# Kernel optimization log

Measured on AMD Instinct MI355X. Metric: run time of the kernel, lower is better.

## Reference

```python
import jax, jax.numpy as jnp
import numpy as np

B, S, D = 4, 2048, 1024
H = 16
HD = D // H  # head_dim = 64


def setup_inputs() -> dict:
    key = jax.random.key(0)
    ks = jax.random.split(key, 8)
    scale = 1.0 / np.sqrt(D)
    return {
        "X_Q": jax.random.normal(ks[0], (B, S, D), dtype=jnp.float32),
        "X_KV": jax.random.normal(ks[1], (B, S, D), dtype=jnp.float32),
        # q_proj: Linear(D, D), weights stored as (in, out)
        "q_w": jax.random.normal(ks[2], (D, D), dtype=jnp.float32) * scale,
        "q_b": jax.random.normal(ks[3], (D,), dtype=jnp.float32) * scale,
        # kv_proj: Linear(D, 2*D)
        "kv_w": jax.random.normal(ks[4], (D, 2 * D), dtype=jnp.float32) * scale,
        "kv_b": jax.random.normal(ks[5], (2 * D,), dtype=jnp.float32) * scale,
        # out_proj: Linear(D, D) (query_dim == input_dim)
        "out_w": jax.random.normal(ks[6], (D, D), dtype=jnp.float32) * scale,
        "out_b": jax.random.normal(ks[7], (D,), dtype=jnp.float32) * scale,
    }


def reference(X_Q, X_KV, q_w, q_b, kv_w, kv_b, out_w, out_b):
    # projections
    q = X_Q @ q_w + q_b                      # [b, s, D]
    kv = X_KV @ kv_w + kv_b                  # [b, l, 2D]
    k, v = jnp.split(kv, 2, axis=-1)         # each [b, l, D]

    def split_heads(t):
        b, m, _ = t.shape
        return t.reshape(b, m, H, HD).transpose(0, 2, 1, 3)  # [b, h, m, d]

    q, k, v = split_heads(q), split_heads(k), split_heads(v)

    # standard attention: full SxL scores (non-flash path)
    scores = jnp.einsum("bhsd,bhld->bhsl", q, k) / np.sqrt(HD)
    attn = jax.nn.softmax(scores, axis=-1)   # dropout_p = 0 -> identity
    out = jnp.einsum("bhsl,bhld->bhsd", attn, v)

    # merge heads: [b, h, s, d] -> [b, s, h*d]
    out = out.transpose(0, 2, 1, 3).reshape(B, S, D)
    return out @ out_w + out_b
```

## Files before the change

kernel.cpp:

```cpp
#include <hip/hip_runtime.h>
#include <hip/hip_bf16.h>
#include <math.h>

#define B_  4
#define S_  2048
#define D_  1024
#define H_  16
#define HD_ 64

typedef __bf16 bf16;
typedef __bf16 bf16x4 __attribute__((ext_vector_type(4)));
typedef __bf16 bf16x8 __attribute__((ext_vector_type(8)));
typedef float  floatx4 __attribute__((ext_vector_type(4)));
typedef unsigned short ushort8 __attribute__((ext_vector_type(8)));

#define QSCALE 0.18033688011112042f

__global__ __launch_bounds__(256) void cast_f32_bf16(
    const float* __restrict__ in, bf16* __restrict__ out, int n) {
  int i = (blockIdx.x * blockDim.x + threadIdx.x) * 4;
  if (i >= n) return;
  float4 v = *reinterpret_cast<const float4*>(in + i);
  bf16x4 o;
  o[0] = (bf16)v.x; o[1] = (bf16)v.y; o[2] = (bf16)v.z; o[3] = (bf16)v.w;
  *reinterpret_cast<bf16x4*>(out + i) = o;
}

__global__ __launch_bounds__(256) void transcast(
    const float* __restrict__ in, bf16* __restrict__ out, int K, int N) {
  __shared__ float tile[32][33];
  int k0 = blockIdx.y * 32, n0 = blockIdx.x * 32;
  int tx = threadIdx.x, ty = threadIdx.y;
  #pragma unroll
  for (int i = ty; i < 32; i += 8)
    tile[i][tx] = in[(size_t)(k0 + i) * N + n0 + tx];
  __syncthreads();
  #pragma unroll
  for (int i = ty; i < 32; i += 8)
    out[(size_t)(n0 + i) * K + k0 + tx] = (bf16)tile[tx][i];
}

template <int MODE>
__global__ __launch_bounds__(256) void gemm_bt(
    const bf16* __restrict__ A, const bf16* __restrict__ Bt,
    const float* __restrict__ bias, void* __restrict__ out,
    int M, int N, int K) {
  __shared__ bf16 As[128][72];
  __shared__ bf16 Bs[128][72];

  const int tid  = threadIdx.x;
  const int m0   = blockIdx.y * 128;
  const int n0   = blockIdx.x * 128;
  const int w    = tid >> 6;
  const int lane = tid & 63;
  const int lr   = lane & 15;
  const int lq   = lane >> 4;
  const int wm   = (w >> 1) * 64;
  const int wn   = (w & 1) * 64;

  floatx4 acc[4][4];
  #pragma unroll
  for (int i = 0; i < 4; i++)
    #pragma unroll
    for (int j = 0; j < 4; j++)
      acc[i][j] = floatx4{0.f, 0.f, 0.f, 0.f};

  const int rA = tid >> 3;
  const int cA = (tid & 7) * 8;

  for (int k0 = 0; k0 < K; k0 += 64) {
    __syncthreads();
    #pragma unroll
    for (int p = 0; p < 4; p++) {
      int r = rA + p * 32;
      *reinterpret_cast<ushort8*>(&As[r][cA]) =
          *reinterpret_cast<const ushort8*>(A + (size_t)(m0 + r) * K + k0 + cA);
      *reinterpret_cast<ushort8*>(&Bs[r][cA]) =
          *reinterpret_cast<const ushort8*>(Bt + (size_t)(n0 + r) * K + k0 + cA);
    }
    __syncthreads();
    #pragma unroll
    for (int kc = 0; kc < 2; kc++) {
      bf16x8 af[4], bfv[4];
      #pragma unroll
      for (int t = 0; t < 4; t++)
        af[t] = *reinterpret_cast<const bf16x8*>(&As[wm + 16 * t + lr][kc * 32 + lq * 8]);
      #pragma unroll
      for (int t = 0; t < 4; t++)
        bfv[t] = *reinterpret_cast<const bf16x8*>(&Bs[wn + 16 * t + lr][kc * 32 + lq * 8]);
      #pragma unroll
      for (int i = 0; i < 4; i++)
        #pragma unroll
        for (int j = 0; j < 4; j++)
          acc[i][j] = __builtin_amdgcn_mfma_f32_16x16x32_bf16(af[i], bfv[j], acc[i][j], 0, 0, 0);
    }
  }

  #pragma unroll
  for (int i = 0; i < 4; i++) {
    int row_base = m0 + wm + 16 * i + lq * 4;
    #pragma unroll
    for (int j = 0; j < 4; j++) {
      int col = n0 + wn + 16 * j + lr;
      float bv = bias[col];
      if (MODE == 2 && col >= 1024) {
        int b = row_base >> 11, s0 = row_base & 2047;
        int c = col - 1024, h = c >> 6, d = c & 63;
        bf16* Vt = (bf16*)out + (size_t)B_ * H_ * S_ * HD_;
        bf16x4 pk;
        #pragma unroll
        for (int r = 0; r < 4; r++) pk[r] = (bf16)(acc[i][j][r] + bv);
        *reinterpret_cast<bf16x4*>(
            &Vt[(((size_t)b * H_ + h) * HD_ + d) * S_ + s0]) = pk;
        continue;
      }
      #pragma unroll
      for (int r = 0; r < 4; r++) {
        int row = row_base + r;
        float v = acc[i][j][r] + bv;
        if (MODE == 0) {
          ((float*)out)[(size_t)row * N + col] = v;
        } else if (MODE == 1) {
          int b = row >> 11, s = row & 2047;
          int h = col >> 6, d = col & 63;
          ((bf16*)out)[(((size_t)b * H_ + h) * S_ + s) * HD_ + d] =
              (bf16)(v * QSCALE);
        } else {
          int b = row >> 11, s = row & 2047;
          int h = col >> 6, d = col & 63;
          ((bf16*)out)[(((size_t)b * H_ + h) * S_ + s) * HD_ + d] = (bf16)v;
        }
      }
    }
  }
}

__global__ __launch_bounds__(256) void attn_kernel(
    const bf16* __restrict__ Q, const bf16* __restrict__ Kb,
    const bf16* __restrict__ Vt, bf16* __restrict__ out) {
  __shared__ bf16 qs[64][72];
  __shared__ bf16 ks[64][72];
  __shared__ bf16 vts[64][72];
  __shared__ bf16 ps[4][16][72];

  const int tid  = threadIdx.x;
  const int w    = tid >> 6;
  const int lane = tid & 63;
  const int lr   = lane & 15;
  const int lq   = lane >> 4;
  const int q0   = blockIdx.x * 64;
  const int bh   = blockIdx.y;
  const size_t base = (size_t)bh * S_ * HD_;

  const int rS = tid >> 3;
  const int cS = (tid & 7) * 8;

  #pragma unroll
  for (int p = 0; p < 2; p++)
    *reinterpret_cast<ushort8*>(&qs[rS + 32 * p][cS]) =
        *reinterpret_cast<const ushort8*>(Q + base + (size_t)(q0 + rS + 32 * p) * HD_ + cS);
  __syncthreads();

  bf16x8 bq[2];
  #pragma unroll
  for (int kc = 0; kc < 2; kc++)
    bq[kc] = *reinterpret_cast<const bf16x8*>(&qs[16 * w + lr][kc * 32 + lq * 8]);

  float l_i = 0.f;
  floatx4 o_acc[4];
  #pragma unroll
  for (int t = 0; t < 4; t++) o_acc[t] = floatx4{0.f, 0.f, 0.f, 0.f};

  for (int l0 = 0; l0 < S_; l0 += 64) {
    __syncthreads();
    #pragma unroll
    for (int p = 0; p < 2; p++) {
      int r = rS + 32 * p;
      *reinterpret_cast<ushort8*>(&ks[r][cS]) =
          *reinterpret_cast<const ushort8*>(Kb + base + (size_t)(l0 + r) * HD_ + cS);
      *reinterpret_cast<ushort8*>(&vts[r][cS]) =
          *reinterpret_cast<const ushort8*>(Vt + base + (size_t)r * S_ + l0 + cS);
    }
    __syncthreads();

    floatx4 sc[4];
    #pragma unroll
    for (int t = 0; t < 4; t++) sc[t] = floatx4{0.f, 0.f, 0.f, 0.f};
    #pragma unroll
    for (int kc = 0; kc < 2; kc++) {
      #pragma unroll
      for (int t = 0; t < 4; t++) {
        bf16x8 ak = *reinterpret_cast<const bf16x8*>(&ks[16 * t + lr][kc * 32 + lq * 8]);
        sc[t] = __builtin_amdgcn_mfma_f32_16x16x32_bf16(ak, bq[kc], sc[t], 0, 0, 0);
      }
    }

    float lsum = 0.f;
    #pragma unroll
    for (int t = 0; t < 4; t++) {
      bf16x4 pk;
      #pragma unroll
      for (int r = 0; r < 4; r++) {
        float p = __builtin_amdgcn_exp2f(sc[t][r]);
        lsum += p;
        pk[r] = (bf16)p;
      }
      *reinterpret_cast<bf16x4*>(&ps[w][lr][16 * t + lq * 4]) = pk;
    }
    l_i += lsum;
    __builtin_amdgcn_wave_barrier();

    #pragma unroll
    for (int kc = 0; kc < 2; kc++) {
      bf16x8 bp = *reinterpret_cast<const bf16x8*>(&ps[w][lr][kc * 32 + lq * 8]);
      #pragma unroll
      for (int t = 0; t < 4; t++) {
        bf16x8 av = *reinterpret_cast<const bf16x8*>(&vts[16 * t + lr][kc * 32 + lq * 8]);
        o_acc[t] = __builtin_amdgcn_mfma_f32_16x16x32_bf16(av, bp, o_acc[t], 0, 0, 0);
      }
    }
  }

  l_i += __shfl_xor(l_i, 16, 64);
  l_i += __shfl_xor(l_i, 32, 64);
  float inv = 1.0f / l_i;

  const int b = bh >> 4, h = bh & 15;
  const int qrow = q0 + 16 * w + lr;
  bf16* orow = out + ((size_t)b * S_ + qrow) * D_ + h * HD_;
  #pragma unroll
  for (int t = 0; t < 4; t++) {
    bf16x4 pk;
    #pragma unroll
    for (int r = 0; r < 4; r++) pk[r] = (bf16)(o_acc[t][r] * inv);
    *reinterpret_cast<bf16x4*>(&orow[16 * t + lq * 4]) = pk;
  }
}

extern "C" void kernel_launch(void* const* d_in, const int* in_sizes, int n_in,
                              void* d_out, int out_size, void* d_ws, size_t ws_size,
                              hipStream_t stream) {
  const float* X_Q   = (const float*)d_in[0];
  const float* X_KV  = (const float*)d_in[1];
  const float* q_w   = (const float*)d_in[2];
  const float* q_b   = (const float*)d_in[3];
  const float* kv_w  = (const float*)d_in[4];
  const float* kv_b  = (const float*)d_in[5];
  const float* out_w = (const float*)d_in[6];
  const float* out_b = (const float*)d_in[7];
  float* out = (float*)d_out;

  char* ws = (char*)d_ws;
  const size_t MB = 1024 * 1024;
  bf16* Xq   = (bf16*)(ws + 0);
  bf16* Xkv  = (bf16*)(ws + 16 * MB);
  bf16* Qb   = (bf16*)(ws + 32 * MB);
  bf16* Kb   = (bf16*)(ws + 48 * MB);
  bf16* qwT  = (bf16*)(ws + 80 * MB);
  bf16* kvwT = (bf16*)(ws + 82 * MB);
  bf16* owT  = (bf16*)(ws + 86 * MB);
  bf16* Vt   = Kb + (size_t)B_ * H_ * S_ * HD_;
  bf16* attn = Xq;

  const int nX = B_ * S_ * D_;

  cast_f32_bf16<<<nX / 1024, 256, 0, stream>>>(X_Q, Xq, nX);
  cast_f32_bf16<<<nX / 1024, 256, 0, stream>>>(X_KV, Xkv, nX);
  transcast<<<dim3(32, 32), dim3(32, 8), 0, stream>>>(q_w, qwT, 1024, 1024);
  transcast<<<dim3(64, 32), dim3(32, 8), 0, stream>>>(kv_w, kvwT, 1024, 2048);
  transcast<<<dim3(32, 32), dim3(32, 8), 0, stream>>>(out_w, owT, 1024, 1024);

  gemm_bt<1><<<dim3(8, 64), 256, 0, stream>>>(Xq, qwT, q_b, Qb, 8192, 1024, 1024);
  gemm_bt<2><<<dim3(16, 64), 256, 0, stream>>>(Xkv, kvwT, kv_b, Kb, 8192, 2048, 1024);
  attn_kernel<<<dim3(32, 64), 256, 0, stream>>>(Qb, Kb, Vt, attn);
  gemm_bt<0><<<dim3(8, 64), 256, 0, stream>>>(attn, owT, out_b, out, 8192, 1024, 1024);
}
```

Baseline: 373.0 us.

## Use direct global-to-LDS loads with XOR swizzle and 128-query attention tiles

Both the GEMM and attention kernels now load global data straight into LDS with global_load_lds, which skips the register round trip. LDS tiles drop their padding and use an XOR swizzle to avoid bank conflicts. The attention kernel now handles 128 query rows per block, two 16-row groups per wave, so each K/V tile feeds twice the MFMA work. It also reuses the Q smem region as the per-wave P buffer and adds a launch-bounds occupancy hint. The risks are more register pressure and that the synchronisation of the async loads relies only on __syncthreads.

Result: faster. 336.9 us (-9.7%).

```diff
diff --git a/kernel.cpp b/kernel.cpp
--- a/kernel.cpp
+++ b/kernel.cpp
@@ -15,6 +15,12 @@
 typedef unsigned short ushort8 __attribute__((ext_vector_type(8)));
 
 #define QSCALE 0.18033688011112042f
+
+__device__ __forceinline__ void async_load16(const bf16* g, bf16* l) {
+  __builtin_amdgcn_global_load_lds(
+      (const __attribute__((address_space(1))) void*)g,
+      (__attribute__((address_space(3))) void*)l, 16, 0, 0);
+}
 
 __global__ __launch_bounds__(256) void cast_f32_bf16(
     const float* __restrict__ in, bf16* __restrict__ out, int n) {
@@ -45,8 +51,8 @@
     const bf16* __restrict__ A, const bf16* __restrict__ Bt,
     const float* __restrict__ bias, void* __restrict__ out,
     int M, int N, int K) {
-  __shared__ bf16 As[128][72];
-  __shared__ bf16 Bs[128][72];
+  __shared__ bf16 As[128][64];
+  __shared__ bf16 Bs[128][64];
 
   const int tid  = threadIdx.x;
   const int m0   = blockIdx.y * 128;
@@ -58,6 +64,11 @@
   const int wm   = (w >> 1) * 64;
   const int wn   = (w & 1) * 64;
 
+  const int srow = lane >> 3;
+  const int sg   = (lane & 7) ^ srow;
+  const bf16* aptr = A  + (size_t)(m0 + 32 * w + srow) * K + 8 * sg;
+  const bf16* bptr = Bt + (size_t)(n0 + 32 * w + srow) * K + 8 * sg;
+
   floatx4 acc[4][4];
   #pragma unroll
   for (int i = 0; i < 4; i++)
@@ -65,29 +76,24 @@
     for (int j = 0; j < 4; j++)
       acc[i][j] = floatx4{0.f, 0.f, 0.f, 0.f};
 
-  const int rA = tid >> 3;
-  const int cA = (tid & 7) * 8;
-
   for (int k0 = 0; k0 < K; k0 += 64) {
     __syncthreads();
     #pragma unroll
     for (int p = 0; p < 4; p++) {
-      int r = rA + p * 32;
-      *reinterpret_cast<ushort8*>(&As[r][cA]) =
-          *reinterpret_cast<const ushort8*>(A + (size_t)(m0 + r) * K + k0 + cA);
-      *reinterpret_cast<ushort8*>(&Bs[r][cA]) =
-          *reinterpret_cast<const ushort8*>(Bt + (size_t)(n0 + r) * K + k0 + cA);
+      async_load16(aptr + (size_t)8 * p * K + k0, &As[32 * w + 8 * p][0]);
+      async_load16(bptr + (size_t)8 * p * K + k0, &Bs[32 * w + 8 * p][0]);
     }
     __syncthreads();
     #pragma unroll
     for (int kc = 0; kc < 2; kc++) {
+      const int sw = 8 * ((kc * 4 + lq) ^ (lr & 7));
       bf16x8 af[4], bfv[4];
       #pragma unroll
       for (int t = 0; t < 4; t++)
-        af[t] = *reinterpret_cast<const bf16x8*>(&As[wm + 16 * t + lr][kc * 32 + lq * 8]);
+        af[t] = *reinterpret_cast<const bf16x8*>(&As[wm + 16 * t + lr][sw]);
       #pragma unroll
       for (int t = 0; t < 4; t++)
-        bfv[t] = *reinterpret_cast<const bf16x8*>(&Bs[wn + 16 * t + lr][kc * 32 + lq * 8]);
+        bfv[t] = *reinterpret_cast<const bf16x8*>(&Bs[wn + 16 * t + lr][sw]);
       #pragma unroll
       for (int i = 0; i < 4; i++)
         #pragma unroll
@@ -135,105 +141,140 @@
   }
 }
 
-__global__ __launch_bounds__(256) void attn_kernel(
+__global__ __launch_bounds__(256, 4) void attn_kernel(
     const bf16* __restrict__ Q, const bf16* __restrict__ Kb,
     const bf16* __restrict__ Vt, bf16* __restrict__ out) {
-  __shared__ bf16 qs[64][72];
-  __shared__ bf16 ks[64][72];
-  __shared__ bf16 vts[64][72];
-  __shared__ bf16 ps[4][16][72];
+  __shared__ bf16 smem[128 * 64 + 64 * 64 + 64 * 64];
+  bf16 (*qs)[64]  = (bf16(*)[64])smem;
+  bf16 (*ks)[64]  = (bf16(*)[64])(smem + 128 * 64);
+  bf16 (*vts)[64] = (bf16(*)[64])(smem + 128 * 64 + 64 * 64);
 
   const int tid  = threadIdx.x;
   const int w    = tid >> 6;
   const int lane = tid & 63;
   const int lr   = lane & 15;
   const int lq   = lane >> 4;
-  const int q0   = blockIdx.x * 64;
+  const int q0   = blockIdx.x * 128;
   const int bh   = blockIdx.y;
   const size_t base = (size_t)bh * S_ * HD_;
 
-  const int rS = tid >> 3;
-  const int cS = (tid & 7) * 8;
-
-  #pragma unroll
-  for (int p = 0; p < 2; p++)
-    *reinterpret_cast<ushort8*>(&qs[rS + 32 * p][cS]) =
-        *reinterpret_cast<const ushort8*>(Q + base + (size_t)(q0 + rS + 32 * p) * HD_ + cS);
+  bf16 (*pw)[64] = (bf16(*)[64])(smem + w * 2048);
+
+  const int srow = lane >> 3;
+  const int sg   = (lane & 7) ^ srow;
+
+  const bf16* qsrc = Q  + base + (size_t)(q0 + 32 * w + srow) * HD_ + 8 * sg;
+  #pragma unroll
+  for (int p = 0; p < 4; p++)
+    async_load16(qsrc + (size_t)8 * p * HD_, &qs[32 * w + 8 * p][0]);
+
+  const bf16* kptr = Kb + base + (size_t)(16 * w + srow) * HD_ + 8 * sg;
+  const bf16* vptr = Vt + base + (size_t)(16 * w + srow) * S_  + 8 * sg;
+
+  #pragma unroll
+  for (int p = 0; p < 2; p++) {
+    async_load16(kptr + (size_t)8 * p * HD_, &ks[16 * w + 8 * p][0]);
+    async_load16(vptr + (size_t)8 * p * S_,  &vts[16 * w + 8 * p][0]);
+  }
   __syncthreads();
 
-  bf16x8 bq[2];
-  #pragma unroll
-  for (int kc = 0; kc < 2; kc++)
-    bq[kc] = *reinterpret_cast<const bf16x8*>(&qs[16 * w + lr][kc * 32 + lq * 8]);
-
-  float l_i = 0.f;
-  floatx4 o_acc[4];
-  #pragma unroll
-  for (int t = 0; t < 4; t++) o_acc[t] = floatx4{0.f, 0.f, 0.f, 0.f};
-
-  for (int l0 = 0; l0 < S_; l0 += 64) {
-    __syncthreads();
-    #pragma unroll
-    for (int p = 0; p < 2; p++) {
-      int r = rS + 32 * p;
-      *reinterpret_cast<ushort8*>(&ks[r][cS]) =
-          *reinterpret_cast<const ushort8*>(Kb + base + (size_t)(l0 + r) * HD_ + cS);
-      *reinterpret_cast<ushort8*>(&vts[r][cS]) =
-          *reinterpret_cast<const ushort8*>(Vt + base + (size_t)r * S_ + l0 + cS);
-    }
-    __syncthreads();
-
-    floatx4 sc[4];
-    #pragma unroll
-    for (int t = 0; t < 4; t++) sc[t] = floatx4{0.f, 0.f, 0.f, 0.f};
+  const int sw0 = 8 * ((0 + lq) ^ (lr & 7));
+  const int sw1 = 8 * ((4 + lq) ^ (lr & 7));
+  bf16x8 bq[2][2];
+  #pragma unroll
+  for (int grp = 0; grp < 2; grp++) {
+    bq[grp][0] = *reinterpret_cast<const bf16x8*>(&qs[32 * w + 16 * grp + lr][sw0]);
+    bq[grp][1] = *reinterpret_cast<const bf16x8*>(&qs[32 * w + 16 * grp + lr][sw1]);
+  }
+
+  float l_i[2] = {0.f, 0.f};
+  floatx4 o_acc[2][4];
+  #pragma unroll
+  for (int grp = 0; grp < 2; grp++)
+    #pragma unroll
+    for (int t = 0; t < 4; t++) o_acc[grp][t] = floatx4{0.f, 0.f, 0.f, 0.f};
+
+  const int NIT = S_ / 64;
+  for (int it = 0; it < NIT; it++) {
+    floatx4 sc[2][4];
+    #pragma unroll
+    for (int grp = 0; grp < 2; grp++)
+      #pragma unroll
+      for (int t = 0; t < 4; t++) sc[grp][t] = floatx4{0.f, 0.f, 0.f, 0.f};
     #pragma unroll
     for (int kc = 0; kc < 2; kc++) {
+      const int sw = kc ? sw1 : sw0;
       #pragma unroll
       for (int t = 0; t < 4; t++) {
-        bf16x8 ak = *reinterpret_cast<const bf16x8*>(&ks[16 * t + lr][kc * 32 + lq * 8]);
-        sc[t] = __builtin_amdgcn_mfma_f32_16x16x32_bf16(ak, bq[kc], sc[t], 0, 0, 0);
-      }
-    }
-
-    float lsum = 0.f;
+        bf16x8 ak = *reinterpret_cast<const bf16x8*>(&ks[16 * t + lr][sw]);
+        sc[0][t] = __builtin_amdgcn_mfma_f32_16x16x32_bf16(ak, bq[0][kc], sc[0][t], 0, 0, 0);
+        sc[1][t] = __builtin_amdgcn_mfma_f32_16x16x32_bf16(ak, bq[1][kc], sc[1][t], 0, 0, 0);
+      }
+    }
+
+    #pragma unroll
+    for (int grp = 0; grp < 2; grp++) {
+      float lsum = 0.f;
+      #pragma unroll
+      for (int t = 0; t < 4; t++) {
+        bf16x4 pk;
+        #pragma unroll
+        for (int r = 0; r < 4; r++) {
+          float p = __builtin_amdgcn_exp2f(sc[grp][t][r]);
+          lsum += p;
+          pk[r] = (bf16)p;
+        }
+        int col = 8 * ((2 * t + (lq >> 1)) ^ (lr & 7)) + 4 * (lq & 1);
+        *reinterpret_cast<bf16x4*>(&pw[16 * grp + lr][col]) = pk;
+      }
+      l_i[grp] += lsum;
+    }
+    __builtin_amdgcn_wave_barrier();
+
+    #pragma unroll
+    for (int kc = 0; kc < 2; kc++) {
+      const int sw = kc ? sw1 : sw0;
+      bf16x8 bp0 = *reinterpret_cast<const bf16x8*>(&pw[lr][sw]);
+      bf16x8 bp1 = *reinterpret_cast<const bf16x8*>(&pw[16 + lr][sw]);
+      #pragma unroll
+      for (int t = 0; t < 4; t++) {
+        bf16x8 av = *reinterpret_cast<const bf16x8*>(&vts[16 * t + lr][sw]);
+        o_acc[0][t] = __builtin_amdgcn_mfma_f32_16x16x32_bf16(av, bp0, o_acc[0][t], 0, 0, 0);
+        o_acc[1][t] = __builtin_amdgcn_mfma_f32_16x16x32_bf16(av, bp1, o_acc[1][t], 0, 0, 0);
+      }
+    }
+
+    if (it + 1 < NIT) {
+      __syncthreads();
+      const int l0n = (it + 1) * 64;
+      #pragma unroll
+      for (int p = 0; p < 2; p++) {
+        async_load16(kptr + (size_t)(l0n + 8 * p) * HD_, &ks[16 * w + 8 * p][0]);
+        async_load16(vptr + (size_t)8 * p * S_ + l0n,    &vts[16 * w + 8 * p][0]);
+      }
+      __syncthreads();
+    }
+  }
+
+  #pragma unroll
+  for (int grp = 0; grp < 2; grp++) {
+    l_i[grp] += __shfl_xor(l_i[grp], 16, 64);
+    l_i[grp] += __shfl_xor(l_i[grp], 32, 64);
+  }
+
+  const int b = bh >> 4, h = bh & 15;
+  #pragma unroll
+  for (int grp = 0; grp < 2; grp++) {
+    const float inv = 1.0f / l_i[grp];
+    const int qrow = q0 + 32 * w + 16 * grp + lr;
+    bf16* orow = out + ((size_t)b * S_ + qrow) * D_ + h * HD_;
     #pragma unroll
     for (int t = 0; t < 4; t++) {
       bf16x4 pk;
       #pragma unroll
-      for (int r = 0; r < 4; r++) {
-        float p = __builtin_amdgcn_exp2f(sc[t][r]);
-        lsum += p;
-        pk[r] = (bf16)p;
-      }
-      *reinterpret_cast<bf16x4*>(&ps[w][lr][16 * t + lq * 4]) = pk;
-    }
-    l_i += lsum;
-    __builtin_amdgcn_wave_barrier();
-
-    #pragma unroll
-    for (int kc = 0; kc < 2; kc++) {
-      bf16x8 bp = *reinterpret_cast<const bf16x8*>(&ps[w][lr][kc * 32 + lq * 8]);
-      #pragma unroll
-      for (int t = 0; t < 4; t++) {
-        bf16x8 av = *reinterpret_cast<const bf16x8*>(&vts[16 * t + lr][kc * 32 + lq * 8]);
-        o_acc[t] = __builtin_amdgcn_mfma_f32_16x16x32_bf16(av, bp, o_acc[t], 0, 0, 0);
-      }
-    }
-  }
-
-  l_i += __shfl_xor(l_i, 16, 64);
-  l_i += __shfl_xor(l_i, 32, 64);
-  float inv = 1.0f / l_i;
-
-  const int b = bh >> 4, h = bh & 15;
-  const int qrow = q0 + 16 * w + lr;
-  bf16* orow = out + ((size_t)b * S_ + qrow) * D_ + h * HD_;
-  #pragma unroll
-  for (int t = 0; t < 4; t++) {
-    bf16x4 pk;
-    #pragma unroll
-    for (int r = 0; r < 4; r++) pk[r] = (bf16)(o_acc[t][r] * inv);
-    *reinterpret_cast<bf16x4*>(&orow[16 * t + lq * 4]) = pk;
+      for (int r = 0; r < 4; r++) pk[r] = (bf16)(o_acc[grp][t][r] * inv);
+      *reinterpret_cast<bf16x4*>(&orow[16 * t + lq * 4]) = pk;
+    }
   }
 }
 
@@ -272,6 +313,6 @@
 
   gemm_bt<1><<<dim3(8, 64), 256, 0, stream>>>(Xq, qwT, q_b, Qb, 8192, 1024, 1024);
   gemm_bt<2><<<dim3(16, 64), 256, 0, stream>>>(Xkv, kvwT, kv_b, Kb, 8192, 2048, 1024);
-  attn_kernel<<<dim3(32, 64), 256, 0, stream>>>(Qb, Kb, Vt, attn);
+  attn_kernel<<<dim3(16, 64), 256, 0, stream>>>(Qb, Kb, Vt, attn);
   gemm_bt<0><<<dim3(8, 64), 256, 0, stream>>>(attn, owT, out_b, out, 8192, 1024, 1024);
 }
```
